# Performance work log

Hardware: AMD Instinct MI355X
Metric: run time of the kernel (lower is better)

Reference implementation:

```python
import jax, jax.numpy as jnp
import numpy as np

W, BS, IN_DIM, H = 512, 64, 1024, 256  # seq len, batch, input dim, d_model


def _gru_direction(x, Wih, Whh, bih, bhh):
    """x: (T, B, in_dim). Returns (outputs (T,B,H), final hidden (B,H)).
    PyTorch GRU gate math with gate order [r, z, n]."""
    Hd = Whh.shape[1]
    gx = jnp.einsum('tbi,gi->tbg', x, Wih) + bih  # (T, B, 3H) precomputed input gates
    h0 = jnp.zeros((x.shape[1], Hd), dtype=x.dtype)

    def step(h, gx_t):
        gh = h @ Whh.T + bhh  # (B, 3H)
        r = jax.nn.sigmoid(gx_t[:, :Hd] + gh[:, :Hd])
        z = jax.nn.sigmoid(gx_t[:, Hd:2 * Hd] + gh[:, Hd:2 * Hd])
        n = jnp.tanh(gx_t[:, 2 * Hd:] + r * gh[:, 2 * Hd:])
        h_new = (1.0 - z) * n + z * h
        return h_new, h_new

    hT, ys = jax.lax.scan(step, h0, gx)
    return ys, hT


def setup_inputs() -> dict:
    key = jax.random.key(0)
    ks = jax.random.split(key, 14)
    s = 1.0 / np.sqrt(H)
    u = lambda k, shape: jax.random.uniform(k, shape, jnp.float32, -s, s)
    return {
        'src': jax.random.normal(ks[0], (W, BS, IN_DIM), jnp.float32),
        # forward-direction GRU params
        'Wih_f': u(ks[1], (3 * H, IN_DIM)), 'Whh_f': u(ks[2], (3 * H, H)),
        'bih_f': u(ks[3], (3 * H,)), 'bhh_f': u(ks[4], (3 * H,)),
        # backward-direction GRU params
        'Wih_b': u(ks[5], (3 * H, IN_DIM)), 'Whh_b': u(ks[6], (3 * H, H)),
        'bih_b': u(ks[7], (3 * H,)), 'bhh_b': u(ks[8], (3 * H,)),
        # projections
        'Wout': u(ks[9], (H, 2 * H)), 'bout': u(ks[10], (H,)),
        'Whid': u(ks[11], (H, 2 * H)), 'bhid': u(ks[12], (H,)),
    }


def reference(src, Wih_f, Whh_f, bih_f, bhh_f, Wih_b, Whh_b, bih_b, bhh_b,
              Wout, bout, Whid, bhid):
    out_f, h_f = _gru_direction(src, Wih_f, Whh_f, bih_f, bhh_f)
    out_b_rev, h_b = _gru_direction(src[::-1], Wih_b, Whh_b, bih_b, bhh_b)
    out_b = out_b_rev[::-1]
    outputs = jnp.concatenate([out_f, out_b], axis=-1)        # (W, BS, 2H)
    outputs = outputs @ Wout.T + bout                          # (W, BS, H)
    hidden = jnp.concatenate([h_f, h_b], axis=-1)[None]        # (1, BS, 2H)
    hidden = jnp.tanh(hidden @ Whid.T + bhid)                  # (1, BS, H)
    return outputs, hidden
```

## Files before the change

kernel.cpp:

```cpp
#include <hip/hip_runtime.h>


typedef short    bf16x8 __attribute__((ext_vector_type(8)));
typedef float    f32x4  __attribute__((ext_vector_type(4)));
typedef float    f32x16 __attribute__((ext_vector_type(16)));

union U16x8 { uint4 u4; bf16x8 b; };

__device__ __forceinline__ unsigned short f2bf(float f) {
  unsigned int u = __builtin_bit_cast(unsigned int, f);
  u += 0x7fffu + ((u >> 16) & 1u);
  return (unsigned short)(u >> 16);
}
__device__ __forceinline__ float bf2f_lo(unsigned int u) {
  return __builtin_bit_cast(float, u << 16);
}
__device__ __forceinline__ float bf2f_hi(unsigned int u) {
  return __builtin_bit_cast(float, u & 0xffff0000u);
}
__device__ __forceinline__ unsigned int cvt_pk_bf16(float lo, float hi) {
  unsigned int r;
  asm("v_cvt_pk_bf16_f32 %0, %1, %2" : "=v"(r) : "v"(lo), "v"(hi));
  return r;
}
__device__ __forceinline__ float fast_rcp(float x) { return __builtin_amdgcn_rcpf(x); }
__device__ __forceinline__ float sigf(float x) { return fast_rcp(1.f + __expf(-x)); }
__device__ __forceinline__ float tanh_fast(float x) {
  float e = __expf(2.f * x);
  return 1.f - 2.f * fast_rcp(e + 1.f);
}

__device__ __forceinline__ void gl_lds16(const char* g, char* l) {
  __builtin_amdgcn_global_load_lds(
      (const __attribute__((address_space(1))) unsigned int*)g,
      (__attribute__((address_space(3))) unsigned int*)l, 16, 0, 0);
}

#define WS_GX      ((size_t)0)
#define WS_OUT     ((size_t)50331648)
#define WS_WIH     ((size_t)67108864)
#define WS_WHH     ((size_t)68681728)
#define WS_WOUT    ((size_t)69074944)
#define WS_WHID    ((size_t)69206016)
#define WS_HFIN    ((size_t)69337088)

__global__ void prep_cvt(const float* __restrict__ wih_f, const float* __restrict__ wih_b,
                         const float* __restrict__ whh_f, const float* __restrict__ whh_b,
                         const float* __restrict__ wout,  const float* __restrict__ whid,
                         unsigned short* __restrict__ dwih, unsigned short* __restrict__ dwhh,
                         unsigned short* __restrict__ dwout, unsigned short* __restrict__ dwhid) {
  int i4 = blockIdx.x * 256 + threadIdx.x;
  const float* s; unsigned short* d;
  if      (i4 < 196608) { s = wih_f; d = dwih; }
  else if (i4 < 393216) { s = wih_b; d = dwih + 786432; i4 -= 196608; }
  else if (i4 < 442368) { s = whh_f; d = dwhh;          i4 -= 393216; }
  else if (i4 < 491520) { s = whh_b; d = dwhh + 196608; i4 -= 442368; }
  else if (i4 < 524288) { s = wout;  d = dwout;         i4 -= 491520; }
  else                  { s = whid;  d = dwhid;         i4 -= 524288; }
  float4 v = ((const float4*)s)[i4];
  ushort4 o; o.x = f2bf(v.x); o.y = f2bf(v.y); o.z = f2bf(v.z); o.w = f2bf(v.w);
  ((ushort4*)d)[i4] = o;
}

__global__ __launch_bounds__(512) void gemm_gx(
    const float* __restrict__ src, const unsigned short* __restrict__ wihbf,
    const float* __restrict__ bih_f, const float* __restrict__ bih_b,
    const float* __restrict__ bhh_f, const float* __restrict__ bhh_b,
    unsigned short* __restrict__ gx) {
  __shared__ char Ab[128 * 128];
  __shared__ char Bb[256 * 128];

  const int bx = blockIdx.x;
  const int xcd = bx & 7, chunk = bx >> 3;
  const int mtile = xcd * 32 + chunk / 6;
  const int ntile = chunk % 6;

  const int tid = threadIdx.x;
  const int w = tid >> 6, l = tid & 63;
  const int l31 = l & 31, l5 = l >> 5;
  const int wr = w >> 2, wc = w & 3;

  f32x16 acc[2][2] = {};

  for (int ks = 0; ks < 16; ++ks) {
#pragma unroll
    for (int i = 0; i < 4; ++i) {
      int cc = i * 512 + tid; int row = cc >> 4, c4 = cc & 15;
      float4 v = *(const float4*)(src + (size_t)(mtile * 128 + row) * 1024 + ks * 64 + c4 * 4);
      ushort4 o; o.x = f2bf(v.x); o.y = f2bf(v.y); o.z = f2bf(v.z); o.w = f2bf(v.w);
      *(ushort4*)(Ab + row * 128 + ((c4 * 8) ^ ((row & 7) << 4))) = o;
    }
#pragma unroll
    for (int i = 0; i < 4; ++i) {
      int cc = i * 512 + tid; int row = cc >> 3, c8 = cc & 7;
      uint4 v = *(const uint4*)(wihbf + (size_t)(ntile * 256 + row) * 1024 + ks * 64 + c8 * 8);
      *(uint4*)(Bb + row * 128 + ((c8 * 16) ^ ((row & 7) << 4))) = v;
    }
    __syncthreads();
#pragma unroll
    for (int kb = 0; kb < 4; ++kb) {
      const int kby = kb * 32 + l5 * 16;
      bf16x8 Af[2], Bf[2];
#pragma unroll
      for (int rt = 0; rt < 2; ++rt) {
        int row = wr * 64 + rt * 32 + l31;
        Af[rt] = *(const bf16x8*)(Ab + row * 128 + (kby ^ ((row & 7) << 4)));
      }
#pragma unroll
      for (int ct = 0; ct < 2; ++ct) {
        int nn = wc * 64 + ct * 32 + l31;
        Bf[ct] = *(const bf16x8*)(Bb + nn * 128 + (kby ^ ((nn & 7) << 4)));
      }
#pragma unroll
      for (int rt = 0; rt < 2; ++rt)
#pragma unroll
        for (int ct = 0; ct < 2; ++ct)
          acc[rt][ct] = __builtin_amdgcn_mfma_f32_32x32x16_bf16(Af[rt], Bf[ct], acc[rt][ct], 0, 0, 0);
    }
    __syncthreads();
  }

  const int cgbase = ntile * 256;
  const int d = cgbase >= 768;
  const float* bih = d ? bih_b : bih_f;
  const float* bhh = d ? bhh_b : bhh_f;
#pragma unroll
  for (int ct = 0; ct < 2; ++ct) {
    const int cg = cgbase + wc * 64 + ct * 32 + l31;
    const int c = cg - d * 768;
    const float bias = bih[c] + (c < 512 ? bhh[c] : 0.f);
#pragma unroll
    for (int rt = 0; rt < 2; ++rt) {
#pragma unroll
      for (int r = 0; r < 16; ++r) {
        const int rr = (r & 3) + 8 * (r >> 2) + 4 * l5;
        const int m = mtile * 128 + wr * 64 + rt * 32 + rr;
        gx[(size_t)d * 25165824 + (size_t)m * 768 + c] = f2bf(acc[rt][ct][r] + bias);
      }
    }
  }
}

__global__ __launch_bounds__(512, 2) void recur(
    const unsigned short* __restrict__ whhbf,
    const float* __restrict__ bhh_f, const float* __restrict__ bhh_b,
    const unsigned short* __restrict__ gx,
    unsigned short* __restrict__ outw,
    unsigned short* __restrict__ hfin) {
  __shared__ char hbuf[2][8192];
  __shared__ char gxbuf[2][24576];

  const int tid = threadIdx.x;
  const int w = tid >> 6, l = tid & 63;
  const int l15 = l & 15, l4 = l >> 4;
  const int d = blockIdx.x >> 2;
  const int bsl = (blockIdx.x & 3) << 4;
  const float* bhh = d ? bhh_b : bhh_f;

  bf16x8 Aw[6][8];
#pragma unroll
  for (int j = 0; j < 6; ++j) {
    const int g3 = j >> 1, jt = j & 1;
    const int n = g3 * 256 + w * 32 + jt * 16 + l15;
#pragma unroll
    for (int kb = 0; kb < 8; ++kb) {
      U16x8 u;
      u.u4 = *(const uint4*)(whhbf + (size_t)d * 196608 + (size_t)n * 256 + kb * 32 + l4 * 8);
      Aw[j][kb] = u.b;
    }
  }
  float bhv[2][4];
#pragma unroll
  for (int jt = 0; jt < 2; ++jt)
#pragma unroll
    for (int q = 0; q < 4; ++q)
      bhv[jt][q] = bhh[512 + w * 32 + jt * 16 + l4 * 4 + q];

  float hown[2][4] = {{0.f, 0.f, 0.f, 0.f}, {0.f, 0.f, 0.f, 0.f}};

  int gofs[3];
#pragma unroll
  for (int i = 0; i < 3; ++i) {
    const int a  = i * 8192 + w * 1024 + l * 16;
    const int pr = a / 1536;
    const int pc = (a % 1536) ^ ((pr & 7) << 4);
    gofs[i] = pr * 1536 + pc;
  }

  const int sw2 = (l15 & 7) << 4;
  const int bq0 = l15 * 1536 + ((w * 64 + l4 * 8) ^ sw2);
  const int bq1 = l15 * 1536 + ((w * 64 + 32 + l4 * 8) ^ sw2);
  const int hw0 = l15 * 512 + ((w * 64 + l4 * 8) ^ (l15 << 4));
  const int hw1 = l15 * 512 + ((w * 64 + 32 + l4 * 8) ^ (l15 << 4));
  const int ob2 = (bsl + l15) * 512 + w * 64 + l4 * 8;

  const int gxstep  = d ? -98304 : 98304;
  const int outstep = d ? -32768 : 32768;
  const char* gxsrc = (const char*)(gx + (size_t)d * 25165824 + (size_t)bsl * 768)
                      + (d ? (size_t)511 * 98304 : 0);
  char* outp = (char*)(outw + (size_t)d * 8388608)
               + (d ? (size_t)511 * 32768 : 0);

  {
    uint4 zz; zz.x = 0u; zz.y = 0u; zz.z = 0u; zz.w = 0u;
    *(uint4*)(hbuf[0] + tid * 16) = zz;
  }
#pragma unroll
  for (int i = 0; i < 3; ++i)
    gl_lds16(gxsrc + gofs[i], gxbuf[0] + i * 8192 + w * 1024);
  asm volatile("s_waitcnt vmcnt(0)" ::: "memory");
  __syncthreads();
  gxsrc += gxstep;

  for (int s = 0; s < 512; ++s) {
    const int cur = s & 1;

#pragma unroll
    for (int i = 0; i < 3; ++i)
      gl_lds16(gxsrc + gofs[i], gxbuf[cur ^ 1] + i * 8192 + w * 1024);
    if (s < 510) gxsrc += gxstep;

    f32x4 acc[6];
#pragma unroll
    for (int j = 0; j < 4; ++j) { acc[j][0] = 0.f; acc[j][1] = 0.f; acc[j][2] = 0.f; acc[j][3] = 0.f; }
#pragma unroll
    for (int jt = 0; jt < 2; ++jt) {
      acc[4 + jt][0] = bhv[jt][0]; acc[4 + jt][1] = bhv[jt][1];
      acc[4 + jt][2] = bhv[jt][2]; acc[4 + jt][3] = bhv[jt][3];
    }
    {
      const char* hb = hbuf[cur];
      const int rsw = l15 << 4;
      const int rbase = l15 * 512;
      __builtin_amdgcn_s_setprio(1);
#pragma unroll
      for (int kb = 0; kb < 8; ++kb) {
        bf16x8 Bf = *(const bf16x8*)(hb + rbase + ((kb * 64 + l4 * 16) ^ rsw));
#pragma unroll
        for (int j = 0; j < 6; ++j)
          acc[j] = __builtin_amdgcn_mfma_f32_16x16x32_bf16(Aw[j][kb], Bf, acc[j], 0, 0, 0);
      }
      __builtin_amdgcn_s_setprio(0);
    }

    const char* gb = gxbuf[cur];
    char* hbn = hbuf[cur ^ 1];
#pragma unroll
    for (int jt = 0; jt < 2; ++jt) {
      const char* base = gb + (jt ? bq1 : bq0);
      const uint2 gr = *(const uint2*)(base);
      const uint2 gz = *(const uint2*)(base + 512);
      const uint2 gn = *(const uint2*)(base + 1024);
      const float gxr[4] = { bf2f_lo(gr.x), bf2f_hi(gr.x), bf2f_lo(gr.y), bf2f_hi(gr.y) };
      const float gxz[4] = { bf2f_lo(gz.x), bf2f_hi(gz.x), bf2f_lo(gz.y), bf2f_hi(gz.y) };
      const float gxn[4] = { bf2f_lo(gn.x), bf2f_hi(gn.x), bf2f_lo(gn.y), bf2f_hi(gn.y) };
      float hv[4];
#pragma unroll
      for (int q = 0; q < 4; ++q) {
        const float rg = sigf(gxr[q] + acc[jt][q]);
        const float zg = sigf(gxz[q] + acc[2 + jt][q]);
        const float ng = tanh_fast(fmaf(rg, acc[4 + jt][q], gxn[q]));
        hv[q] = ng + zg * (hown[jt][q] - ng);
        hown[jt][q] = hv[q];
      }
      uint2 P;
      P.x = cvt_pk_bf16(hv[0], hv[1]);
      P.y = cvt_pk_bf16(hv[2], hv[3]);
      *(uint2*)(hbn + (jt ? hw1 : hw0)) = P;
      *(uint2*)(outp + ob2 + jt * 32) = P;
    }
    outp += outstep;

    asm volatile("s_waitcnt lgkmcnt(0)" ::: "memory");
    asm volatile("s_waitcnt vmcnt(2)" ::: "memory");
    __builtin_amdgcn_sched_barrier(0);
    __builtin_amdgcn_s_barrier();
    asm volatile("" ::: "memory");
  }

#pragma unroll
  for (int jt = 0; jt < 2; ++jt) {
    uint2 P;
    P.x = cvt_pk_bf16(hown[jt][0], hown[jt][1]);
    P.y = cvt_pk_bf16(hown[jt][2], hown[jt][3]);
    *(uint2*)(hfin + (size_t)d * 16384 + (size_t)(bsl + l15) * 256
              + w * 32 + jt * 16 + l4 * 4) = P;
  }
}

__global__ __launch_bounds__(256) void gemm_out(
    const unsigned short* __restrict__ outws, const unsigned short* __restrict__ woutbf,
    const float* __restrict__ bout, float* __restrict__ out) {
  __shared__ char Ab[128 * 128];
  __shared__ char Bb[128 * 128];
  const int mtile = blockIdx.x, ntile = blockIdx.y;
  const int tid = threadIdx.x;
  const int w = tid >> 6, l = tid & 63;
  const int l31 = l & 31, l5 = l >> 5;
  const int wr = w >> 1, wc = w & 1;

  f32x16 acc[2][2] = {};

  for (int ks = 0; ks < 8; ++ks) {
    const unsigned short* asrc = outws + (size_t)(ks >> 2) * 8388608;
    const int k0 = (ks & 3) * 64;
#pragma unroll
    for (int i = 0; i < 4; ++i) {
      int cc = i * 256 + tid; int row = cc >> 3, c8 = cc & 7;
      uint4 v = *(const uint4*)(asrc + (size_t)(mtile * 128 + row) * 256 + k0 + c8 * 8);
      *(uint4*)(Ab + row * 128 + ((c8 * 16) ^ ((row & 7) << 4))) = v;
    }
#pragma unroll
    for (int i = 0; i < 4; ++i) {
      int cc = i * 256 + tid; int row = cc >> 3, c8 = cc & 7;
      uint4 v = *(const uint4*)(woutbf + (size_t)(ntile * 128 + row) * 512 + ks * 64 + c8 * 8);
      *(uint4*)(Bb + row * 128 + ((c8 * 16) ^ ((row & 7) << 4))) = v;
    }
    __syncthreads();
#pragma unroll
    for (int kb = 0; kb < 4; ++kb) {
      const int kby = kb * 32 + l5 * 16;
      bf16x8 Af[2], Bf[2];
#pragma unroll
      for (int rt = 0; rt < 2; ++rt) {
        int row = wr * 64 + rt * 32 + l31;
        Af[rt] = *(const bf16x8*)(Ab + row * 128 + (kby ^ ((row & 7) << 4)));
      }
#pragma unroll
      for (int ct = 0; ct < 2; ++ct) {
        int nn = wc * 64 + ct * 32 + l31;
        Bf[ct] = *(const bf16x8*)(Bb + nn * 128 + (kby ^ ((nn & 7) << 4)));
      }
#pragma unroll
      for (int rt = 0; rt < 2; ++rt)
#pragma unroll
        for (int ct = 0; ct < 2; ++ct)
          acc[rt][ct] = __builtin_amdgcn_mfma_f32_32x32x16_bf16(Af[rt], Bf[ct], acc[rt][ct], 0, 0, 0);
    }
    __syncthreads();
  }

#pragma unroll
  for (int ct = 0; ct < 2; ++ct) {
    const int n = ntile * 128 + wc * 64 + ct * 32 + l31;
    const float bias = bout[n];
#pragma unroll
    for (int rt = 0; rt < 2; ++rt) {
#pragma unroll
      for (int r = 0; r < 16; ++r) {
        const int rr = (r & 3) + 8 * (r >> 2) + 4 * l5;
        const int m = mtile * 128 + wr * 64 + rt * 32 + rr;
        out[(size_t)m * 256 + n] = acc[rt][ct][r] + bias;
      }
    }
  }
}

__global__ __launch_bounds__(256) void hidden_k(
    const unsigned short* __restrict__ hfin, const unsigned short* __restrict__ whidbf,
    const float* __restrict__ bhid, float* __restrict__ out) {
  __shared__ char Ab[64 * 1024];
  const int tid = threadIdx.x;
  const int w = tid >> 6, l = tid & 63;
  const int l31 = l & 31, l5 = l >> 5;

#pragma unroll
  for (int i = 0; i < 16; ++i) {
    int cc = i * 256 + tid; int row = cc >> 6, c16 = cc & 63;
    int k = c16 * 8; int dsel = k >= 256;
    uint4 v = *(const uint4*)(hfin + dsel * 16384 + row * 256 + (k & 255));
    *(uint4*)(Ab + row * 1024 + ((c16 * 16) ^ ((row & 7) << 4))) = v;
  }
  __syncthreads();

  f32x16 acc[2][2] = {};
#pragma unroll 4
  for (int kb = 0; kb < 32; ++kb) {
    const int kby = kb * 32 + l5 * 16;
    bf16x8 Af[2], Bf[2];
#pragma unroll
    for (int rt = 0; rt < 2; ++rt) {
      int row = rt * 32 + l31;
      Af[rt] = *(const bf16x8*)(Ab + row * 1024 + (kby ^ ((row & 7) << 4)));
    }
#pragma unroll
    for (int ct = 0; ct < 2; ++ct) {
      int n = w * 64 + ct * 32 + l31;
      U16x8 u; u.u4 = *(const uint4*)(whidbf + (size_t)n * 512 + kb * 16 + l5 * 8);
      Bf[ct] = u.b;
    }
#pragma unroll
    for (int rt = 0; rt < 2; ++rt)
#pragma unroll
      for (int ct = 0; ct < 2; ++ct)
        acc[rt][ct] = __builtin_amdgcn_mfma_f32_32x32x16_bf16(Af[rt], Bf[ct], acc[rt][ct], 0, 0, 0);
  }

#pragma unroll
  for (int ct = 0; ct < 2; ++ct) {
    const int n = w * 64 + ct * 32 + l31;
    const float bias = bhid[n];
#pragma unroll
    for (int rt = 0; rt < 2; ++rt) {
#pragma unroll
      for (int r = 0; r < 16; ++r) {
        const int rr = (r & 3) + 8 * (r >> 2) + 4 * l5;
        const int b = rt * 32 + rr;
        out[8388608 + (size_t)b * 256 + n] = tanh_fast(acc[rt][ct][r] + bias);
      }
    }
  }
}

extern "C" void kernel_launch(void* const* d_in, const int* in_sizes, int n_in,
                              void* d_out, int out_size, void* d_ws, size_t ws_size,
                              hipStream_t stream) {
  const float* src   = (const float*)d_in[0];
  const float* wih_f = (const float*)d_in[1];
  const float* whh_f = (const float*)d_in[2];
  const float* bih_f = (const float*)d_in[3];
  const float* bhh_f = (const float*)d_in[4];
  const float* wih_b = (const float*)d_in[5];
  const float* whh_b = (const float*)d_in[6];
  const float* bih_b = (const float*)d_in[7];
  const float* bhh_b = (const float*)d_in[8];
  const float* wout  = (const float*)d_in[9];
  const float* bout  = (const float*)d_in[10];
  const float* whid  = (const float*)d_in[11];
  const float* bhid  = (const float*)d_in[12];

  unsigned short* ws     = (unsigned short*)d_ws;
  unsigned short* gx     = ws + WS_GX;
  unsigned short* outw   = ws + WS_OUT;
  unsigned short* wihbf  = ws + WS_WIH;
  unsigned short* whhbf  = ws + WS_WHH;
  unsigned short* woutbf = ws + WS_WOUT;
  unsigned short* whidbf = ws + WS_WHID;
  unsigned short* hfin   = ws + WS_HFIN;
  float* out = (float*)d_out;

  prep_cvt<<<2176, 256, 0, stream>>>(wih_f, wih_b, whh_f, whh_b, wout, whid,
                                     wihbf, whhbf, woutbf, whidbf);
  gemm_gx<<<1536, 512, 0, stream>>>(src, wihbf, bih_f, bih_b, bhh_f, bhh_b, gx);
  recur<<<8, 512, 0, stream>>>(whhbf, bhh_f, bhh_b, gx, outw, hfin);
  gemm_out<<<dim3(256, 2), 256, 0, stream>>>(outw, woutbf, bout, out);
  hidden_k<<<1, 256, 0, stream>>>(hfin, whidbf, bhid, out);
}
```

Before: 1.700 ms.

## Split GRU recurrence across 16 waves per block, halving per-wave hidden tiles

```diff
diff --git a/kernel.cpp b/kernel.cpp
--- a/kernel.cpp
+++ b/kernel.cpp
@@ -34,6 +34,10 @@
   __builtin_amdgcn_global_load_lds(
       (const __attribute__((address_space(1))) unsigned int*)g,
       (__attribute__((address_space(3))) unsigned int*)l, 16, 0, 0);
+}
+
+__device__ __forceinline__ int gxsw(int r) {
+  return ((r & 3) << 5) | ((r & 4) << 2);
 }
 
 #define WS_GX      ((size_t)0)
@@ -141,7 +145,7 @@
   }
 }
 
-__global__ __launch_bounds__(512, 2) void recur(
+__global__ __launch_bounds__(1024, 4) void recur(
     const unsigned short* __restrict__ whhbf,
     const float* __restrict__ bhh_f, const float* __restrict__ bhh_b,
     const unsigned short* __restrict__ gx,
@@ -157,42 +161,34 @@
   const int bsl = (blockIdx.x & 3) << 4;
   const float* bhh = d ? bhh_b : bhh_f;
 
-  bf16x8 Aw[6][8];
-#pragma unroll
-  for (int j = 0; j < 6; ++j) {
-    const int g3 = j >> 1, jt = j & 1;
-    const int n = g3 * 256 + w * 32 + jt * 16 + l15;
+  bf16x8 Aw[3][8];
+#pragma unroll
+  for (int g = 0; g < 3; ++g) {
+    const int n = g * 256 + w * 16 + l15;
 #pragma unroll
     for (int kb = 0; kb < 8; ++kb) {
       U16x8 u;
       u.u4 = *(const uint4*)(whhbf + (size_t)d * 196608 + (size_t)n * 256 + kb * 32 + l4 * 8);
-      Aw[j][kb] = u.b;
-    }
-  }
-  float bhv[2][4];
-#pragma unroll
-  for (int jt = 0; jt < 2; ++jt)
-#pragma unroll
-    for (int q = 0; q < 4; ++q)
-      bhv[jt][q] = bhh[512 + w * 32 + jt * 16 + l4 * 4 + q];
-
-  float hown[2][4] = {{0.f, 0.f, 0.f, 0.f}, {0.f, 0.f, 0.f, 0.f}};
-
-  int gofs[3];
-#pragma unroll
-  for (int i = 0; i < 3; ++i) {
-    const int a  = i * 8192 + w * 1024 + l * 16;
-    const int pr = a / 1536;
-    const int pc = (a % 1536) ^ ((pr & 7) << 4);
-    gofs[i] = pr * 1536 + pc;
-  }
-
-  const int sw2 = (l15 & 7) << 4;
-  const int bq0 = l15 * 1536 + ((w * 64 + l4 * 8) ^ sw2);
-  const int bq1 = l15 * 1536 + ((w * 64 + 32 + l4 * 8) ^ sw2);
-  const int hw0 = l15 * 512 + ((w * 64 + l4 * 8) ^ (l15 << 4));
-  const int hw1 = l15 * 512 + ((w * 64 + 32 + l4 * 8) ^ (l15 << 4));
-  const int ob2 = (bsl + l15) * 512 + w * 64 + l4 * 8;
+      Aw[g][kb] = u.b;
+    }
+  }
+  float bhv[4];
+#pragma unroll
+  for (int q = 0; q < 4; ++q)
+    bhv[q] = bhh[512 + w * 16 + l4 * 4 + q];
+
+  float hown[4] = {0.f, 0.f, 0.f, 0.f};
+
+  const int a0 = w * 1024 + l * 16;
+  const int pr0 = a0 / 1536;
+  const int gofs0 = pr0 * 1536 + ((a0 % 1536) ^ gxsw(pr0));
+  const int a1 = 16384 + w * 1024 + l * 16;
+  const int pr1 = a1 / 1536;
+  const int gofs1 = pr1 * 1536 + ((a1 % 1536) ^ gxsw(pr1));
+
+  const int bq = l15 * 1536 + ((w * 32 + l4 * 8) ^ gxsw(l15));
+  const int hw = l15 * 512 + ((w * 32 + l4 * 8) ^ (l15 << 4));
+  const int ob = (bsl + l15) * 512 + w * 32 + l4 * 8;
 
   const int gxstep  = d ? -98304 : 98304;
   const int outstep = d ? -32768 : 32768;
@@ -201,13 +197,12 @@
   char* outp = (char*)(outw + (size_t)d * 8388608)
                + (d ? (size_t)511 * 32768 : 0);
 
-  {
+  if (tid < 512) {
     uint4 zz; zz.x = 0u; zz.y = 0u; zz.z = 0u; zz.w = 0u;
     *(uint4*)(hbuf[0] + tid * 16) = zz;
   }
-#pragma unroll
-  for (int i = 0; i < 3; ++i)
-    gl_lds16(gxsrc + gofs[i], gxbuf[0] + i * 8192 + w * 1024);
+  gl_lds16(gxsrc + gofs0, gxbuf[0] + w * 1024);
+  if (w < 8) gl_lds16(gxsrc + gofs1, gxbuf[0] + 16384 + w * 1024);
   asm volatile("s_waitcnt vmcnt(0)" ::: "memory");
   __syncthreads();
   gxsrc += gxstep;
@@ -215,19 +210,14 @@
   for (int s = 0; s < 512; ++s) {
     const int cur = s & 1;
 
-#pragma unroll
-    for (int i = 0; i < 3; ++i)
-      gl_lds16(gxsrc + gofs[i], gxbuf[cur ^ 1] + i * 8192 + w * 1024);
+    gl_lds16(gxsrc + gofs0, gxbuf[cur ^ 1] + w * 1024);
+    if (w < 8) gl_lds16(gxsrc + gofs1, gxbuf[cur ^ 1] + 16384 + w * 1024);
     if (s < 510) gxsrc += gxstep;
 
-    f32x4 acc[6];
-#pragma unroll
-    for (int j = 0; j < 4; ++j) { acc[j][0] = 0.f; acc[j][1] = 0.f; acc[j][2] = 0.f; acc[j][3] = 0.f; }
-#pragma unroll
-    for (int jt = 0; jt < 2; ++jt) {
-      acc[4 + jt][0] = bhv[jt][0]; acc[4 + jt][1] = bhv[jt][1];
-      acc[4 + jt][2] = bhv[jt][2]; acc[4 + jt][3] = bhv[jt][3];
-    }
+    f32x4 acc[3];
+    acc[0][0] = 0.f; acc[0][1] = 0.f; acc[0][2] = 0.f; acc[0][3] = 0.f;
+    acc[1][0] = 0.f; acc[1][1] = 0.f; acc[1][2] = 0.f; acc[1][3] = 0.f;
+    acc[2][0] = bhv[0]; acc[2][1] = bhv[1]; acc[2][2] = bhv[2]; acc[2][3] = bhv[3];
     {
       const char* hb = hbuf[cur];
       const int rsw = l15 << 4;
@@ -237,17 +227,16 @@
       for (int kb = 0; kb < 8; ++kb) {
         bf16x8 Bf = *(const bf16x8*)(hb + rbase + ((kb * 64 + l4 * 16) ^ rsw));
 #pragma unroll
-        for (int j = 0; j < 6; ++j)
-          acc[j] = __builtin_amdgcn_mfma_f32_16x16x32_bf16(Aw[j][kb], Bf, acc[j], 0, 0, 0);
+        for (int g = 0; g < 3; ++g)
+          acc[g] = __builtin_amdgcn_mfma_f32_16x16x32_bf16(Aw[g][kb], Bf, acc[g], 0, 0, 0);
       }
       __builtin_amdgcn_s_setprio(0);
     }
 
     const char* gb = gxbuf[cur];
     char* hbn = hbuf[cur ^ 1];
-#pragma unroll
-    for (int jt = 0; jt < 2; ++jt) {
-      const char* base = gb + (jt ? bq1 : bq0);
+    {
+      const char* base = gb + bq;
       const uint2 gr = *(const uint2*)(base);
       const uint2 gz = *(const uint2*)(base + 512);
       const uint2 gn = *(const uint2*)(base + 1024);
@@ -257,34 +246,33 @@
       float hv[4];
 #pragma unroll
       for (int q = 0; q < 4; ++q) {
-        const float rg = sigf(gxr[q] + acc[jt][q]);
-        const float zg = sigf(gxz[q] + acc[2 + jt][q]);
-        const float ng = tanh_fast(fmaf(rg, acc[4 + jt][q], gxn[q]));
-        hv[q] = ng + zg * (hown[jt][q] - ng);
-        hown[jt][q] = hv[q];
+        const float rg = sigf(gxr[q] + acc[0][q]);
+        const float zg = sigf(gxz[q] + acc[1][q]);
+        const float ng = tanh_fast(fmaf(rg, acc[2][q], gxn[q]));
+        hv[q] = ng + zg * (hown[q] - ng);
+        hown[q] = hv[q];
       }
       uint2 P;
       P.x = cvt_pk_bf16(hv[0], hv[1]);
       P.y = cvt_pk_bf16(hv[2], hv[3]);
-      *(uint2*)(hbn + (jt ? hw1 : hw0)) = P;
-      *(uint2*)(outp + ob2 + jt * 32) = P;
+      *(uint2*)(hbn + hw) = P;
+      *(uint2*)(outp + ob) = P;
     }
     outp += outstep;
 
     asm volatile("s_waitcnt lgkmcnt(0)" ::: "memory");
-    asm volatile("s_waitcnt vmcnt(2)" ::: "memory");
+    asm volatile("s_waitcnt vmcnt(1)" ::: "memory");
     __builtin_amdgcn_sched_barrier(0);
     __builtin_amdgcn_s_barrier();
     asm volatile("" ::: "memory");
   }
 
-#pragma unroll
-  for (int jt = 0; jt < 2; ++jt) {
+  {
     uint2 P;
-    P.x = cvt_pk_bf16(hown[jt][0], hown[jt][1]);
-    P.y = cvt_pk_bf16(hown[jt][2], hown[jt][3]);
+    P.x = cvt_pk_bf16(hown[0], hown[1]);
+    P.y = cvt_pk_bf16(hown[2], hown[3]);
     *(uint2*)(hfin + (size_t)d * 16384 + (size_t)(bsl + l15) * 256
-              + w * 32 + jt * 16 + l4 * 4) = P;
+              + w * 16 + l4 * 4) = P;
   }
 }
 
@@ -442,7 +430,7 @@
   prep_cvt<<<2176, 256, 0, stream>>>(wih_f, wih_b, whh_f, whh_b, wout, whid,
                                      wihbf, whhbf, woutbf, whidbf);
   gemm_gx<<<1536, 512, 0, stream>>>(src, wihbf, bih_f, bih_b, bhh_f, bhh_b, gx);
-  recur<<<8, 512, 0, stream>>>(whhbf, bhh_f, bhh_b, gx, outw, hfin);
+  recur<<<8, 1024, 0, stream>>>(whhbf, bhh_f, bhh_b, gx, outw, hfin);
   gemm_out<<<dim3(256, 2), 256, 0, stream>>>(outw, woutbf, bout, out);
   hidden_k<<<1, 256, 0, stream>>>(hfin, whidbf, bhid, out);
 }
```

New measurement: 2.147 ms. 26.3% more time.
